# Kernel tuning notes

Measured on AMD Instinct MI355X. Metric: run time of the kernel, lower is better.

## Reference

```python
import jax, jax.numpy as jnp
import numpy as np

NUM_HEADS = 4
NUM_GROUPS = 8
EPS = 1e-5


def setup_inputs() -> dict:
    key = jax.random.key(0)
    ks = jax.random.split(key, 4)
    B, C, H, W = 4, 256, 64, 64
    x = jax.random.normal(ks[0], (B, C, H, W), dtype=jnp.float32)
    gamma = jnp.ones((C,), dtype=jnp.float32)
    beta = jnp.zeros((C,), dtype=jnp.float32)
    w_qkv = jax.random.normal(ks[1], (3 * C, C), dtype=jnp.float32) * 0.02
    b_qkv = jnp.zeros((3 * C,), dtype=jnp.float32)
    w_proj = jax.random.normal(ks[2], (C, C), dtype=jnp.float32) * 0.02
    b_proj = jnp.zeros((C,), dtype=jnp.float32)
    return {"x": x, "gamma": gamma, "beta": beta, "w_qkv": w_qkv,
            "b_qkv": b_qkv, "w_proj": w_proj, "b_proj": b_proj}


def _group_norm(x, gamma, beta):
    B, C, H, W = x.shape
    xg = x.reshape(B, NUM_GROUPS, C // NUM_GROUPS, H, W)
    mean = xg.mean(axis=(2, 3, 4), keepdims=True)
    var = xg.var(axis=(2, 3, 4), keepdims=True)
    xn = ((xg - mean) * jax.lax.rsqrt(var + EPS)).reshape(B, C, H, W)
    return xn * gamma[None, :, None, None] + beta[None, :, None, None]


def reference(x, gamma, beta, w_qkv, b_qkv, w_proj, b_proj):
    B, C, H, W = x.shape
    d = C // NUM_HEADS
    scale = d ** (-0.5)
    xn = _group_norm(x, gamma, beta)
    # 1x1 conv == per-pixel linear: (B,C,H,W) x (3C,C) -> (B,3C,H,W)
    qkv = jnp.einsum('bchw,oc->bohw', xn, w_qkv) + b_qkv[None, :, None, None]
    q, k, v = jnp.split(qkv, 3, axis=1)
    S = H * W
    q = q.reshape(B, NUM_HEADS, d, S)  # (B,h,d,S)
    k = k.reshape(B, NUM_HEADS, d, S)
    v = v.reshape(B, NUM_HEADS, d, S)
    # attn scores: q^T k, scaled AFTER the matmul (as in source)
    attn = jax.nn.softmax(jnp.einsum('bhds,bhdt->bhst', q, k) * scale, axis=-1)
    # out = attn @ v^T -> (B,h,S,d) then transpose to (B,h,d,S) -> (B,C,H,W)
    out = jnp.einsum('bhst,bhdt->bhds', attn, v).reshape(B, C, H, W)
    y = jnp.einsum('bchw,oc->bohw', out, w_proj) + b_proj[None, :, None, None]
    return x + y
```

## Files before the change

### kernel.cpp

```cpp
#include <hip/hip_runtime.h>
#include <hip/hip_bf16.h>


typedef __attribute__((ext_vector_type(8))) short          b16x8;
typedef __attribute__((ext_vector_type(4))) float          f32x4;
typedef __attribute__((ext_vector_type(4))) unsigned short u16x4;
typedef __attribute__((ext_vector_type(8))) unsigned short u16x8;

#define SWZ(row, chunk) (((chunk) ^ ((row) & 7)))

__device__ __forceinline__ unsigned short f2bf(float f) {
    union { float f; unsigned u; } v; v.f = f;
    unsigned r = v.u + 0x7FFF + ((v.u >> 16) & 1);
    return (unsigned short)(r >> 16);
}

__device__ __forceinline__ float bf2f(unsigned short u) {
    union { unsigned u; float f; } v; v.u = ((unsigned)u) << 16;
    return v.f;
}

__device__ __forceinline__ unsigned bfpack_trunc(float lo, float hi) {
    union { float f; unsigned u; } a, b;
    a.f = hi; b.f = lo;
    return __builtin_amdgcn_perm(a.u, b.u, 0x07060302u);
}

__device__ __forceinline__ float fexp2(float x) {
#if __has_builtin(__builtin_amdgcn_exp2f)
    return __builtin_amdgcn_exp2f(x);
#else
    return exp2f(x);
#endif
}

__device__ __forceinline__ float frcp(float x) {
#if __has_builtin(__builtin_amdgcn_rcpf)
    return __builtin_amdgcn_rcpf(x);
#else
    return 1.f / x;
#endif
}

__device__ __forceinline__ void gll16(const void* g, void* l) {
    __builtin_amdgcn_global_load_lds(
        (const __attribute__((address_space(1))) unsigned int*)g,
        (__attribute__((address_space(3))) unsigned int*)l, 16, 0, 0);
}

__global__ __launch_bounds__(256) void gn_prepack(const float* __restrict__ x,
                                                  float* __restrict__ partials,
                                                  const float* __restrict__ wqkv,
                                                  const float* __restrict__ bqkv,
                                                  unsigned short* __restrict__ wsw,
                                                  float* __restrict__ bq_pre) {
    int bx = blockIdx.x;
    int t = threadIdx.x;
    if (bx < 512) {
        int bg = bx >> 4, part = bx & 15;
        const float* xp = x + (size_t)bg * 131072 + (size_t)part * 8192;
        float s = 0.f, ss = 0.f;
        for (int k = 0; k < 8; k++) {
            float4 v = *(const float4*)(xp + t * 4 + k * 1024);
            s += v.x + v.y + v.z + v.w;
            ss += v.x * v.x + v.y * v.y + v.z * v.z + v.w * v.w;
        }
        for (int off = 32; off; off >>= 1) {
            s += __shfl_down(s, off);
            ss += __shfl_down(ss, off);
        }
        __shared__ float rs[4], rss[4];
        if ((t & 63) == 0) { rs[t >> 6] = s; rss[t >> 6] = ss; }
        __syncthreads();
        if (t == 0) {
            partials[2 * bx]     = rs[0] + rs[1] + rs[2] + rs[3];
            partials[2 * bx + 1] = rss[0] + rss[1] + rss[2] + rss[3];
        }
    } else {
        int gid = (bx - 512) * 256 + t;
        const float qs = 0.125f * 1.44269504f;
        int o = gid >> 5, ch = gid & 31, cblk = ch >> 3, chl = ch & 7;
        float sc = (o < 256) ? qs : 1.f;
        const float* src = &wqkv[o * 256 + ch * 8];
        u16x8 v;
        for (int i = 0; i < 8; i++) v[i] = f2bf(src[i] * sc);
        *(u16x8*)&wsw[((cblk * 768 + o) << 6) + SWZ(o, chl) * 8] = v;
        if (gid < 768) bq_pre[gid] = bqkv[gid] * ((gid < 256) ? qs : 1.f);
    }
}

__global__ __launch_bounds__(256) void qkv_gemm(const float* __restrict__ x,
                                                const float* __restrict__ gamma,
                                                const float* __restrict__ beta,
                                                const unsigned short* __restrict__ wsw,
                                                const float* __restrict__ bq_pre,
                                                const float* __restrict__ partials,
                                                unsigned short* __restrict__ qT,
                                                unsigned short* __restrict__ kT,
                                                unsigned short* __restrict__ vT) {
    __shared__ __align__(16) unsigned short Asm[256 * 64];
    __shared__ __align__(16) unsigned short Bsm[64 * 72];
    __shared__ float stats_s[16];
    int s0 = blockIdx.x * 64, sec = blockIdx.y, b = blockIdx.z;
    int t = threadIdx.x, lane = t & 63, wv = t >> 6;
    int l15 = lane & 15, quad = lane >> 4;
    f32x4 acc[4][4] = {};

    if (t < 8) {
        float s = 0.f, ss = 0.f;
        for (int p = 0; p < 16; p++) {
            s  += partials[2 * ((b * 8 + t) * 16 + p)];
            ss += partials[2 * ((b * 8 + t) * 16 + p) + 1];
        }
        const float invN = 1.f / 131072.f;
        float mean = s * invN;
        float var = ss * invN - mean * mean;
        stats_s[2 * t] = mean;
        stats_s[2 * t + 1] = rsqrtf(var + 1e-5f);
    }

    int tc = t >> 5;
    int ts = (t & 31) * 2;

    for (int k0 = 0; k0 < 256; k0 += 64) {
        int cblk = k0 >> 6;
        __syncthreads();
        const unsigned short* asrc = wsw + (((size_t)cblk * 768 + sec * 256) << 6);
        for (int j = 0; j < 8; j++) {
            int blk = wv * 8 + j;
            gll16(asrc + blk * 512 + lane * 8, &Asm[blk * 512]);
        }
        {
            int cbase = k0 + tc * 8;
            int g = cbase >> 5;
            float mean = stats_s[2 * g], rstd = stats_s[2 * g + 1];
            u16x8 r0, r1;
            for (int ci = 0; ci < 8; ci++) {
                int c = cbase + ci;
                float2 xv = *(const float2*)&x[((size_t)(b * 256 + c)) * 4096 + s0 + ts];
                float ga = gamma[c] * rstd, be = beta[c] - mean * gamma[c] * rstd;
                r0[ci] = (short)f2bf(xv.x * ga + be);
                r1[ci] = (short)f2bf(xv.y * ga + be);
            }
            *(u16x8*)&Bsm[(ts + 0) * 72 + tc * 8] = r0;
            *(u16x8*)&Bsm[(ts + 1) * 72 + tc * 8] = r1;
        }
        __syncthreads();
        for (int kc = 0; kc < 2; kc++) {
            b16x8 bb[4];
            for (int nn = 0; nn < 4; nn++)
                bb[nn] = *(const b16x8*)(Bsm + (nn * 16 + l15) * 72 + kc * 32 + quad * 8);
            for (int ot = 0; ot < 4; ot++) {
                int row = wv * 16 + l15;
                b16x8 a = *(const b16x8*)&Asm[(ot * 64 + row) * 64 + SWZ(row, kc * 4 + quad) * 8];
                for (int nn = 0; nn < 4; nn++)
                    acc[ot][nn] = __builtin_amdgcn_mfma_f32_16x16x32_bf16(a, bb[nn], acc[ot][nn], 0, 0, 0);
            }
        }
    }

    if (sec < 2) {
        unsigned short* dstT = (sec == 0) ? qT : kT;
        for (int ot = 0; ot < 4; ot++) {
            __syncthreads();
            for (int nn = 0; nn < 4; nn++) {
                u16x4 pv;
                for (int r = 0; r < 4; r++) {
                    int o = sec * 256 + ot * 64 + wv * 16 + quad * 4 + r;
                    pv[r] = f2bf(acc[ot][nn][r] + bq_pre[o]);
                }
                *(u16x4*)&Bsm[(nn * 16 + l15) * 72 + wv * 16 + quad * 4] = pv;
            }
            __syncthreads();
            unsigned short* dst = dstT + (size_t)(b * 4 + ot) * 4096 * 64;
            int s_l = t >> 2;
            for (int j = 0; j < 2; j++) {
                int cp = (t & 3) * 2 + j;
                u16x8 val = *(u16x8*)&Bsm[s_l * 72 + cp * 8];
                *(u16x8*)&dst[(size_t)(s0 + s_l) * 64 + SWZ(s_l, cp) * 8] = val;
            }
        }
    } else {
        int kt = blockIdx.x;
        for (int ot = 0; ot < 4; ot++) {
            int bh = b * 4 + ot;
            for (int r = 0; r < 4; r++) {
                int dd = wv * 16 + quad * 4 + r;
                float bs = bq_pre[512 + ot * 64 + dd];
                u16x4 pv = { f2bf(acc[ot][0][r] + bs), f2bf(acc[ot][1][r] + bs),
                             f2bf(acc[ot][2][r] + bs), f2bf(acc[ot][3][r] + bs) };
                size_t off = ((size_t)(bh * 64 + kt) * 64 + dd) * 64
                           + SWZ(dd, l15 >> 1) * 8 + (l15 & 1) * 4;
                *(u16x4*)&vT[off] = pv;
            }
        }
    }
}

__global__ __launch_bounds__(256) void attn_kernel(const unsigned short* __restrict__ qT,
                                                   const unsigned short* __restrict__ kT,
                                                   const unsigned short* __restrict__ vT,
                                                   unsigned short* __restrict__ Opart,
                                                   float* __restrict__ lsum) {
    __shared__ __align__(16) unsigned short QP[128 * 64];
    __shared__ __align__(16) unsigned short Ksm[2][64 * 64];
    __shared__ __align__(16) unsigned short Vsm[64 * 64];
    int bx = blockIdx.x;
    int q0 = (bx >> 1) * 128;
    int half = bx & 1;
    int kt0 = half * 32, ktN = kt0 + 32;
    int h = blockIdx.y, b = blockIdx.z;
    int bh = b * 4 + h, slab = bh * 2 + half;
    int t = threadIdx.x, lane = t & 63, wv = t >> 6;
    int l15 = lane & 15, quad = lane >> 4;

    const unsigned short* qTb = qT + (size_t)bh * 4096 * 64;
    const unsigned short* kTb = kT + (size_t)bh * 4096 * 64;
    const unsigned short* vTb = vT + (size_t)bh * 64 * 4096;

    for (int j = 0; j < 8; j++) {
        int i = wv + 4 * j;
        if (i < 16) {
            gll16(qTb + (size_t)q0 * 64 + i * 512 + lane * 8, &QP[i * 512]);
        } else if (i < 24) {
            int ii = i - 16;
            gll16(kTb + (size_t)kt0 * 4096 + ii * 512 + lane * 8, &Ksm[0][ii * 512]);
        } else {
            int ii = i - 24;
            gll16(vTb + (size_t)kt0 * 4096 + ii * 512 + lane * 8, &Vsm[ii * 512]);
        }
    }
    __syncthreads();

    b16x8 aq[2][2];
    for (int mt = 0; mt < 2; mt++)
        for (int kc = 0; kc < 2; kc++) {
            int row = wv * 32 + mt * 16 + l15;
            aq[mt][kc] = *(const b16x8*)&QP[row * 64 + SWZ(row, kc * 4 + quad) * 8];
        }

    b16x8 ones;
    for (int i = 0; i < 8; i++) ones[i] = (short)0x3F80;

    f32x4 O[2][4] = {};
    f32x4 lsacc[2] = {};

    for (int kt = kt0; kt < ktN; kt++) {
        int cur = kt & 1;
        int nb = cur ^ 1;
        u16x8 vpre0, vpre1;
        bool more = (kt < ktN - 1);
        if (more) {
            for (int j = 0; j < 2; j++) {
                int blk = wv * 2 + j;
                gll16(kTb + (size_t)(kt + 1) * 4096 + blk * 512 + lane * 8,
                      &Ksm[nb][blk * 512]);
            }
            const unsigned short* vsrc = vTb + (size_t)(kt + 1) * 4096;
            vpre0 = *(const u16x8*)&vsrc[t * 8];
            vpre1 = *(const u16x8*)&vsrc[2048 + t * 8];
        }

        f32x4 sc[2][4] = {};
        for (int kc = 0; kc < 2; kc++) {
            b16x8 bk[4];
            for (int nk = 0; nk < 4; nk++) {
                int row = nk * 16 + l15;
                bk[nk] = *(const b16x8*)&Ksm[cur][row * 64 + SWZ(l15, kc * 4 + quad) * 8];
            }
            for (int mt = 0; mt < 2; mt++)
                for (int nk = 0; nk < 4; nk++)
                    sc[mt][nk] = __builtin_amdgcn_mfma_f32_16x16x32_bf16(
                        aq[mt][kc], bk[nk], sc[mt][nk], 0, 0, 0);
        }

        for (int mt = 0; mt < 2; mt++) {
            for (int r = 0; r < 4; r++) {
                float p0 = fexp2(sc[mt][0][r]);
                float p1 = fexp2(sc[mt][1][r]);
                float p2 = fexp2(sc[mt][2][r]);
                float p3 = fexp2(sc[mt][3][r]);
                int row = wv * 32 + mt * 16 + quad * 4 + r;
                uint2 pk = { bfpack_trunc(p0, p1), bfpack_trunc(p2, p3) };
                *(uint2*)&QP[row * 64 + SWZ(row, l15 >> 1) * 8 + (l15 & 1) * 4] = pk;
            }
        }

        for (int kc = 0; kc < 2; kc++) {
            b16x8 ap[2], bv[4];
            for (int mt = 0; mt < 2; mt++) {
                int row = wv * 32 + mt * 16 + l15;
                ap[mt] = *(const b16x8*)&QP[row * 64 + SWZ(row, kc * 4 + quad) * 8];
            }
            for (int nf = 0; nf < 4; nf++) {
                int row = nf * 16 + l15;
                bv[nf] = *(const b16x8*)&Vsm[row * 64 + SWZ(l15, kc * 4 + quad) * 8];
            }
            for (int mt = 0; mt < 2; mt++) {
                lsacc[mt] = __builtin_amdgcn_mfma_f32_16x16x32_bf16(
                    ap[mt], ones, lsacc[mt], 0, 0, 0);
                for (int nf = 0; nf < 4; nf++)
                    O[mt][nf] = __builtin_amdgcn_mfma_f32_16x16x32_bf16(
                        ap[mt], bv[nf], O[mt][nf], 0, 0, 0);
            }
        }

        __syncthreads();
        if (more) {
            *(u16x8*)&Vsm[t * 8]        = vpre0;
            *(u16x8*)&Vsm[2048 + t * 8] = vpre1;
            __syncthreads();
        }
    }

    for (int mt = 0; mt < 2; mt++)
        for (int r = 0; r < 4; r++) {
            int srow = q0 + wv * 32 + mt * 16 + quad * 4 + r;
            if (l15 == 0) lsum[(size_t)slab * 4096 + srow] = lsacc[mt][r];
        }

    for (int mt = 0; mt < 2; mt++)
        for (int nf = 0; nf < 4; nf++)
            for (int r = 0; r < 4; r++) {
                int s = q0 + wv * 32 + mt * 16 + quad * 4 + r;
                int d = nf * 16 + l15;
                Opart[((size_t)slab * 4096 + s) * 64 + d] = f2bf(O[mt][nf][r]);
            }
}

__global__ __launch_bounds__(256) void proj_gemm(const unsigned short* __restrict__ Opart,
                                                 const float* __restrict__ lsum,
                                                 const float* __restrict__ w,
                                                 const float* __restrict__ bias,
                                                 const float* __restrict__ x,
                                                 float* __restrict__ out) {
    __shared__ __align__(16) unsigned short Asm[64 * 72];
    __shared__ __align__(16) unsigned short Bsm[64 * 72];
    int s0 = blockIdx.x * 64, o0 = blockIdx.y * 64, b = blockIdx.z;
    int t = threadIdx.x, lane = t & 63, wv = t >> 6;
    int l15 = lane & 15, quad = lane >> 4;
    int rl = t >> 2;
    f32x4 acc[4] = {};
    for (int k0 = 0; k0 < 256; k0 += 64) {
        __syncthreads();
        for (int j = 0; j < 4; j++) {
            int c4 = (t & 3) * 16 + j * 4;
            float4 w4 = *(const float4*)&w[(size_t)(o0 + rl) * 256 + k0 + c4];
            u16x4 p = { f2bf(w4.x), f2bf(w4.y), f2bf(w4.z), f2bf(w4.w) };
            *(u16x4*)&Asm[rl * 72 + c4] = p;
        }
        {
            int hh = k0 >> 6;
            int bh = b * 4 + hh;
            int s = s0 + rl;
            float l0 = lsum[(size_t)(bh * 2 + 0) * 4096 + s];
            float l1 = lsum[(size_t)(bh * 2 + 1) * 4096 + s];
            float rcp = frcp(l0 + l1);
            for (int j = 0; j < 2; j++) {
                int off = (t & 3) * 16 + j * 8;
                u16x8 o0v = *(const u16x8*)&Opart[((size_t)(bh * 2 + 0) * 4096 + s) * 64 + off];
                u16x8 o1v = *(const u16x8*)&Opart[((size_t)(bh * 2 + 1) * 4096 + s) * 64 + off];
                u16x8 res;
                for (int i = 0; i < 8; i++)
                    res[i] = f2bf((bf2f(o0v[i]) + bf2f(o1v[i])) * rcp);
                *(u16x8*)&Bsm[rl * 72 + off] = res;
            }
        }
        __syncthreads();
        for (int kc = 0; kc < 2; kc++) {
            b16x8 a = *(const b16x8*)(Asm + (wv * 16 + l15) * 72 + kc * 32 + quad * 8);
            for (int nn = 0; nn < 4; nn++) {
                b16x8 bb = *(const b16x8*)(Bsm + (nn * 16 + l15) * 72 + kc * 32 + quad * 8);
                acc[nn] = __builtin_amdgcn_mfma_f32_16x16x32_bf16(a, bb, acc[nn], 0, 0, 0);
            }
        }
    }
    for (int nn = 0; nn < 4; nn++) {
        for (int r = 0; r < 4; r++) {
            int o = o0 + wv * 16 + quad * 4 + r;
            int s = s0 + nn * 16 + l15;
            size_t idx = ((size_t)(b * 256 + o)) * 4096 + s;
            out[idx] = acc[nn][r] + bias[o] + x[idx];
        }
    }
}

extern "C" void kernel_launch(void* const* d_in, const int* in_sizes, int n_in,
                              void* d_out, int out_size, void* d_ws, size_t ws_size,
                              hipStream_t stream) {
    const float* x      = (const float*)d_in[0];
    const float* gamma  = (const float*)d_in[1];
    const float* beta   = (const float*)d_in[2];
    const float* w_qkv  = (const float*)d_in[3];
    const float* b_qkv  = (const float*)d_in[4];
    const float* w_proj = (const float*)d_in[5];
    const float* b_proj = (const float*)d_in[6];
    float* out = (float*)d_out;

    unsigned short* ws = (unsigned short*)d_ws;
    unsigned short* qT    = ws;
    unsigned short* kT    = qT + (size_t)16 * 4096 * 64;
    unsigned short* vT    = kT + (size_t)16 * 4096 * 64;
    unsigned short* scratch = vT + (size_t)16 * 4096 * 64;
    unsigned short* Opart = scratch + (size_t)4 * 4096 * 256;
    float*          lsump = (float*)(Opart + (size_t)32 * 4096 * 64);
    unsigned short* wqkv_sw = (unsigned short*)lsump;
    float*          bq_pre  = (float*)((char*)lsump + 393216);
    float*          partials = (float*)scratch;

    hipLaunchKernelGGL(gn_prepack,  dim3(608),      dim3(256), 0, stream,
                       x, partials, w_qkv, b_qkv, wqkv_sw, bq_pre);
    hipLaunchKernelGGL(qkv_gemm,    dim3(64, 3, 4), dim3(256), 0, stream,
                       x, gamma, beta, wqkv_sw, bq_pre, partials, qT, kT, vT);
    hipLaunchKernelGGL(attn_kernel, dim3(64, 4, 4), dim3(256), 0, stream,
                       qT, kT, vT, Opart, lsump);
    hipLaunchKernelGGL(proj_gemm,   dim3(64, 4, 4), dim3(256), 0, stream,
                       Opart, lsump, w_proj, b_proj, x, out);
}
```

Measured before the change: 194.8 us.

## Halve attention block to two waves with 64 rows each; prepack proj weights

The attention kernel now runs 128 threads per block, with each wave owning 64 query rows instead of 32. Each K/V tile loaded into shared memory is therefore reused by more MFMA work per wave, though register pressure rises and fewer waves per block are available to hide latency. Separately, the projection weights are converted to bf16 once in the prepack kernel into a swizzled layout. proj_gemm then loads them directly into LDS with global_load_lds instead of converting fp32 per block.

```diff
diff --git a/kernel.cpp b/kernel.cpp
--- a/kernel.cpp
+++ b/kernel.cpp
@@ -53,7 +53,9 @@
                                                   const float* __restrict__ wqkv,
                                                   const float* __restrict__ bqkv,
                                                   unsigned short* __restrict__ wsw,
-                                                  float* __restrict__ bq_pre) {
+                                                  float* __restrict__ bq_pre,
+                                                  const float* __restrict__ wproj,
+                                                  unsigned short* __restrict__ wswp) {
     int bx = blockIdx.x;
     int t = threadIdx.x;
     if (bx < 512) {
@@ -76,7 +78,7 @@
             partials[2 * bx]     = rs[0] + rs[1] + rs[2] + rs[3];
             partials[2 * bx + 1] = rss[0] + rss[1] + rss[2] + rss[3];
         }
-    } else {
+    } else if (bx < 608) {
         int gid = (bx - 512) * 256 + t;
         const float qs = 0.125f * 1.44269504f;
         int o = gid >> 5, ch = gid & 31, cblk = ch >> 3, chl = ch & 7;
@@ -86,6 +88,13 @@
         for (int i = 0; i < 8; i++) v[i] = f2bf(src[i] * sc);
         *(u16x8*)&wsw[((cblk * 768 + o) << 6) + SWZ(o, chl) * 8] = v;
         if (gid < 768) bq_pre[gid] = bqkv[gid] * ((gid < 256) ? qs : 1.f);
+    } else {
+        int gid = (bx - 608) * 256 + t;
+        int o = gid >> 5, ch = gid & 31, cblk = ch >> 3, chl = ch & 7;
+        const float* src = &wproj[o * 256 + ch * 8];
+        u16x8 v;
+        for (int i = 0; i < 8; i++) v[i] = f2bf(src[i]);
+        *(u16x8*)&wswp[((cblk * 256 + o) << 6) + SWZ(o, chl) * 8] = v;
     }
 }
 
@@ -197,11 +206,11 @@
     }
 }
 
-__global__ __launch_bounds__(256) void attn_kernel(const unsigned short* __restrict__ qT,
-                                                   const unsigned short* __restrict__ kT,
-                                                   const unsigned short* __restrict__ vT,
-                                                   unsigned short* __restrict__ Opart,
-                                                   float* __restrict__ lsum) {
+__global__ __launch_bounds__(128, 2) void attn_kernel(const unsigned short* __restrict__ qT,
+                                                      const unsigned short* __restrict__ kT,
+                                                      const unsigned short* __restrict__ vT,
+                                                      unsigned short* __restrict__ Opart,
+                                                      float* __restrict__ lsum) {
     __shared__ __align__(16) unsigned short QP[128 * 64];
     __shared__ __align__(16) unsigned short Ksm[2][64 * 64];
     __shared__ __align__(16) unsigned short Vsm[64 * 64];
@@ -218,8 +227,8 @@
     const unsigned short* kTb = kT + (size_t)bh * 4096 * 64;
     const unsigned short* vTb = vT + (size_t)bh * 64 * 4096;
 
-    for (int j = 0; j < 8; j++) {
-        int i = wv + 4 * j;
+    for (int j = 0; j < 16; j++) {
+        int i = wv + 2 * j;
         if (i < 16) {
             gll16(qTb + (size_t)q0 * 64 + i * 512 + lane * 8, &QP[i * 512]);
         } else if (i < 24) {
@@ -232,71 +241,71 @@
     }
     __syncthreads();
 
-    b16x8 aq[2][2];
-    for (int mt = 0; mt < 2; mt++)
+    b16x8 aq[4][2];
+    for (int mt = 0; mt < 4; mt++)
         for (int kc = 0; kc < 2; kc++) {
-            int row = wv * 32 + mt * 16 + l15;
+            int row = wv * 64 + mt * 16 + l15;
             aq[mt][kc] = *(const b16x8*)&QP[row * 64 + SWZ(row, kc * 4 + quad) * 8];
         }
 
     b16x8 ones;
     for (int i = 0; i < 8; i++) ones[i] = (short)0x3F80;
 
-    f32x4 O[2][4] = {};
-    f32x4 lsacc[2] = {};
+    f32x4 O[4][4] = {};
+    f32x4 lsacc[4] = {};
 
     for (int kt = kt0; kt < ktN; kt++) {
         int cur = kt & 1;
         int nb = cur ^ 1;
-        u16x8 vpre0, vpre1;
+        u16x8 vpre[4];
         bool more = (kt < ktN - 1);
         if (more) {
-            for (int j = 0; j < 2; j++) {
-                int blk = wv * 2 + j;
+            for (int j = 0; j < 4; j++) {
+                int blk = wv * 4 + j;
                 gll16(kTb + (size_t)(kt + 1) * 4096 + blk * 512 + lane * 8,
                       &Ksm[nb][blk * 512]);
             }
             const unsigned short* vsrc = vTb + (size_t)(kt + 1) * 4096;
-            vpre0 = *(const u16x8*)&vsrc[t * 8];
-            vpre1 = *(const u16x8*)&vsrc[2048 + t * 8];
-        }
-
-        f32x4 sc[2][4] = {};
+            for (int j = 0; j < 4; j++)
+                vpre[j] = *(const u16x8*)&vsrc[j * 1024 + t * 8];
+        }
+
+        f32x4 sc[4][4] = {};
         for (int kc = 0; kc < 2; kc++) {
             b16x8 bk[4];
             for (int nk = 0; nk < 4; nk++) {
                 int row = nk * 16 + l15;
                 bk[nk] = *(const b16x8*)&Ksm[cur][row * 64 + SWZ(l15, kc * 4 + quad) * 8];
             }
-            for (int mt = 0; mt < 2; mt++)
+            for (int mt = 0; mt < 4; mt++)
                 for (int nk = 0; nk < 4; nk++)
                     sc[mt][nk] = __builtin_amdgcn_mfma_f32_16x16x32_bf16(
                         aq[mt][kc], bk[nk], sc[mt][nk], 0, 0, 0);
         }
 
-        for (int mt = 0; mt < 2; mt++) {
+        for (int mt = 0; mt < 4; mt++) {
             for (int r = 0; r < 4; r++) {
                 float p0 = fexp2(sc[mt][0][r]);
                 float p1 = fexp2(sc[mt][1][r]);
                 float p2 = fexp2(sc[mt][2][r]);
                 float p3 = fexp2(sc[mt][3][r]);
-                int row = wv * 32 + mt * 16 + quad * 4 + r;
+                int row = wv * 64 + mt * 16 + quad * 4 + r;
                 uint2 pk = { bfpack_trunc(p0, p1), bfpack_trunc(p2, p3) };
                 *(uint2*)&QP[row * 64 + SWZ(row, l15 >> 1) * 8 + (l15 & 1) * 4] = pk;
             }
         }
 
         for (int kc = 0; kc < 2; kc++) {
-            b16x8 ap[2], bv[4];
-            for (int mt = 0; mt < 2; mt++) {
-                int row = wv * 32 + mt * 16 + l15;
+            b16x8 ap[4], bv[4];
+            for (int mt = 0; mt < 4; mt++) {
+                int row = wv * 64 + mt * 16 + l15;
                 ap[mt] = *(const b16x8*)&QP[row * 64 + SWZ(row, kc * 4 + quad) * 8];
             }
             for (int nf = 0; nf < 4; nf++) {
                 int row = nf * 16 + l15;
                 bv[nf] = *(const b16x8*)&Vsm[row * 64 + SWZ(l15, kc * 4 + quad) * 8];
             }
-            for (int mt = 0; mt < 2; mt++) {
+            for (int mt = 0; mt < 4; mt++) {
                 lsacc[mt] = __builtin_amdgcn_mfma_f32_16x16x32_bf16(
                     ap[mt], ones, lsacc[mt], 0, 0, 0);
                 for (int nf = 0; nf < 4; nf++)
@@ -307,22 +316,22 @@
 
         __syncthreads();
         if (more) {
-            *(u16x8*)&Vsm[t * 8]        = vpre0;
-            *(u16x8*)&Vsm[2048 + t * 8] = vpre1;
+            for (int j = 0; j < 4; j++)
+                *(u16x8*)&Vsm[j * 1024 + t * 8] = vpre[j];
             __syncthreads();
         }
     }
 
-    for (int mt = 0; mt < 2; mt++)
+    for (int mt = 0; mt < 4; mt++)
         for (int r = 0; r < 4; r++) {
-            int srow = q0 + wv * 32 + mt * 16 + quad * 4 + r;
+            int srow = q0 + wv * 64 + mt * 16 + quad * 4 + r;
             if (l15 == 0) lsum[(size_t)slab * 4096 + srow] = lsacc[mt][r];
         }
 
-    for (int mt = 0; mt < 2; mt++)
+    for (int mt = 0; mt < 4; mt++)
         for (int nf = 0; nf < 4; nf++)
             for (int r = 0; r < 4; r++) {
-                int s = q0 + wv * 32 + mt * 16 + quad * 4 + r;
+                int s = q0 + wv * 64 + mt * 16 + quad * 4 + r;
                 int d = nf * 16 + l15;
                 Opart[((size_t)slab * 4096 + s) * 64 + d] = f2bf(O[mt][nf][r]);
             }
@@ -330,11 +339,11 @@
 
 __global__ __launch_bounds__(256) void proj_gemm(const unsigned short* __restrict__ Opart,
                                                  const float* __restrict__ lsum,
-                                                 const float* __restrict__ w,
+                                                 const unsigned short* __restrict__ wswp,
                                                  const float* __restrict__ bias,
                                                  const float* __restrict__ x,
                                                  float* __restrict__ out) {
-    __shared__ __align__(16) unsigned short Asm[64 * 72];
+    __shared__ __align__(16) unsigned short Asm[64 * 64];
     __shared__ __align__(16) unsigned short Bsm[64 * 72];
     int s0 = blockIdx.x * 64, o0 = blockIdx.y * 64, b = blockIdx.z;
     int t = threadIdx.x, lane = t & 63, wv = t >> 6;
@@ -342,16 +351,15 @@
     int rl = t >> 2;
     f32x4 acc[4] = {};
     for (int k0 = 0; k0 < 256; k0 += 64) {
-        __syncthreads();
-        for (int j = 0; j < 4; j++) {
-            int c4 = (t & 3) * 16 + j * 4;
-            float4 w4 = *(const float4*)&w[(size_t)(o0 + rl) * 256 + k0 + c4];
-            u16x4 p = { f2bf(w4.x), f2bf(w4.y), f2bf(w4.z), f2bf(w4.w) };
-            *(u16x4*)&Asm[rl * 72 + c4] = p;
+        int cblk = k0 >> 6;
+        __syncthreads();
+        const unsigned short* asrc = wswp + (((size_t)cblk * 256 + o0) << 6);
+        for (int j = 0; j < 2; j++) {
+            int blk = wv * 2 + j;
+            gll16(asrc + blk * 512 + lane * 8, &Asm[blk * 512]);
         }
         {
-            int hh = k0 >> 6;
-            int bh = b * 4 + hh;
+            int bh = b * 4 + cblk;
             int s = s0 + rl;
             float l0 = lsum[(size_t)(bh * 2 + 0) * 4096 + s];
             float l1 = lsum[(size_t)(bh * 2 + 1) * 4096 + s];
@@ -368,7 +376,8 @@
         }
         __syncthreads();
         for (int kc = 0; kc < 2; kc++) {
-            b16x8 a = *(const b16x8*)(Asm + (wv * 16 + l15) * 72 + kc * 32 + quad * 8);
+            int row = wv * 16 + l15;
+            b16x8 a = *(const b16x8*)&Asm[row * 64 + SWZ(row, kc * 4 + quad) * 8];
             for (int nn = 0; nn < 4; nn++) {
                 b16x8 bb = *(const b16x8*)(Bsm + (nn * 16 + l15) * 72 + kc * 32 + quad * 8);
                 acc[nn] = __builtin_amdgcn_mfma_f32_16x16x32_bf16(a, bb, acc[nn], 0, 0, 0);
@@ -407,13 +416,14 @@
     unsigned short* wqkv_sw = (unsigned short*)lsump;
     float*          bq_pre  = (float*)((char*)lsump + 393216);
     float*          partials = (float*)scratch;
-
-    hipLaunchKernelGGL(gn_prepack,  dim3(608),      dim3(256), 0, stream,
-                       x, partials, w_qkv, b_qkv, wqkv_sw, bq_pre);
+    unsigned short* wproj_sw = scratch + 32768;
+
+    hipLaunchKernelGGL(gn_prepack,  dim3(640),      dim3(256), 0, stream,
+                       x, partials, w_qkv, b_qkv, wqkv_sw, bq_pre, w_proj, wproj_sw);
     hipLaunchKernelGGL(qkv_gemm,    dim3(64, 3, 4), dim3(256), 0, stream,
                        x, gamma, beta, wqkv_sw, bq_pre, partials, qT, kT, vT);
-    hipLaunchKernelGGL(attn_kernel, dim3(64, 4, 4), dim3(256), 0, stream,
+    hipLaunchKernelGGL(attn_kernel, dim3(64, 4, 4), dim3(128), 0, stream,
                        qT, kT, vT, Opart, lsump);
     hipLaunchKernelGGL(proj_gemm,   dim3(64, 4, 4), dim3(256), 0, stream,
-                       Opart, lsump, w_proj, b_proj, x, out);
-}
+                       Opart, lsump, wproj_sw, b_proj, x, out);
+}
```

After: 183.0 us. 6.1% less time.
